# Kernel optimization log

Measured on AMD Instinct MI355X. Metric: run time of the kernel, lower is better.

Reference implementation:

```python
import jax, jax.numpy as jnp
import numpy as np

DECAY = 0.99
EPSILON = 1e-05


def setup_inputs() -> dict:
    key = jax.random.key(0)
    k1, k2, k3, k4 = jax.random.split(key, 4)
    B, S, D, K = 16, 2048, 512, 2048
    x = jax.random.normal(k1, (B, S, D), dtype=jnp.float32)
    embed = jax.random.normal(k2, (K, D), dtype=jnp.float32)
    cluster_size = jax.random.uniform(k3, (K,), dtype=jnp.float32)
    embed_avg = jax.random.normal(k4, (K, D), dtype=jnp.float32)
    return {"x": x, "embed": embed, "cluster_size": cluster_size, "embed_avg": embed_avg}


def reference(x, embed, cluster_size, embed_avg):
    # x: [B,S,D]  embed: [K,D]  cluster_size: [K]  embed_avg: [K,D]
    B, S, D = x.shape
    K = embed.shape[0]
    xf = x.reshape(-1, D)  # [N,D], N=B*S

    # quantize(): negative squared euclidean distance, argmax over codebook
    x_sq = jnp.sum(xf * xf, axis=1, keepdims=True)            # [N,1]
    e_sq = jnp.sum(embed * embed, axis=1)[None, :]            # [1,K]
    dist = -(x_sq - 2.0 * (xf @ embed.T) + e_sq)              # [N,K]
    embed_ind = jnp.argmax(dist, axis=-1)                     # [N] int

    # dequantize
    quantize = embed[embed_ind].reshape(B, S, D)

    # training EMA updates (onehot.sum(0) and x^T @ onehot expressed as segment sums)
    ones = jnp.ones((xf.shape[0],), dtype=x.dtype)
    bins = jax.ops.segment_sum(ones, embed_ind, num_segments=K)        # [K] == onehot.sum(0)
    embed_sum_t = jax.ops.segment_sum(xf, embed_ind, num_segments=K)   # [K,D] == (x.T @ onehot).T

    new_cluster_size = cluster_size * DECAY + (1.0 - DECAY) * bins
    new_embed_avg = embed_avg * DECAY + (1.0 - DECAY) * embed_sum_t

    total = new_cluster_size.sum()
    smoothed = (new_cluster_size + EPSILON) / (total + K * EPSILON) * total  # laplace smoothing
    new_embed = new_embed_avg / smoothed[:, None]

    return (quantize,
            embed_ind.reshape(B, S),
            dist.reshape(B, S, K),
            new_cluster_size,
            new_embed_avg,
            new_embed)
```

## Files before the change

### kernel.cpp

```cpp
#include <hip/hip_runtime.h>

#define DECAY 0.99f
#define OMD   0.01f
#define EPS   1e-5f

constexpr int Bb = 16, Ss = 2048, Dd = 512, Kk = 2048;
constexpr int Nn = Bb * Ss;

typedef __attribute__((ext_vector_type(8))) short short8;
typedef __attribute__((ext_vector_type(4))) float f32x4;

__device__ __forceinline__ unsigned short f2bf(float x) {
    unsigned u = __float_as_uint(x);
    unsigned r = (u + 0x7FFFu + ((u >> 16) & 1u)) >> 16;
    return (unsigned short)r;
}
__device__ __forceinline__ float bf2f(unsigned short u) {
    return __uint_as_float((unsigned)u << 16);
}

__device__ __forceinline__ void gload_lds16(const void* g, void* l) {
    __builtin_amdgcn_global_load_lds(
        (const __attribute__((address_space(1))) void*)g,
        (__attribute__((address_space(3))) void*)l, 16, 0, 0);
}

#define BARRIER() do { asm volatile("" ::: "memory"); \
                       __builtin_amdgcn_s_barrier();  \
                       asm volatile("" ::: "memory"); } while (0)

__global__ void rows_sq(const float* __restrict__ in, float* __restrict__ out, int nrows) {
    int row  = blockIdx.x * 4 + (threadIdx.x >> 6);
    int lane = threadIdx.x & 63;
    if (row >= nrows) return;
    const float4* p = (const float4*)(in + (size_t)row * Dd);
    float s = 0.f;
    #pragma unroll
    for (int i = 0; i < 2; ++i) {
        float4 v = p[lane + 64 * i];
        s += v.x * v.x + v.y * v.y + v.z * v.z + v.w * v.w;
    }
    #pragma unroll
    for (int off = 32; off; off >>= 1) s += __shfl_down(s, off);
    if (lane == 0) out[row] = s;
}

__global__ void conv_rows(const float* __restrict__ in,
                          unsigned short* __restrict__ ph,
                          unsigned short* __restrict__ pm,
                          float* __restrict__ sq) {
    int row  = blockIdx.x * 4 + (threadIdx.x >> 6);
    int lane = threadIdx.x & 63;
    const float4* p = (const float4*)(in + (size_t)row * Dd);
    ushort4* h4 = (ushort4*)(ph + (size_t)row * Dd);
    ushort4* m4 = (ushort4*)(pm + (size_t)row * Dd);
    float s = 0.f;
    #pragma unroll
    for (int i = 0; i < 2; ++i) {
        int idx = lane + 64 * i;
        float4 v = p[idx];
        float f[4] = {v.x, v.y, v.z, v.w};
        unsigned short hh[4], mm[4];
        #pragma unroll
        for (int j = 0; j < 4; ++j) {
            float x = f[j];
            s += x * x;
            unsigned short a = f2bf(x);
            unsigned short b = f2bf(x - bf2f(a));
            hh[j] = a; mm[j] = b;
        }
        h4[idx] = make_ushort4(hh[0], hh[1], hh[2], hh[3]);
        m4[idx] = make_ushort4(mm[0], mm[1], mm[2], mm[3]);
    }
    #pragma unroll
    for (int off = 32; off; off >>= 1) s += __shfl_down(s, off);
    if (lane == 0) sq[row] = s;
}

__global__ __launch_bounds__(512, 1) void gemm_split256(
    const unsigned short* __restrict__ xp,
    const unsigned short* __restrict__ ep,
    const float* __restrict__ xsq,
    const float* __restrict__ esq,
    float* __restrict__ dist,
    unsigned long long* __restrict__ packed)
{
    __shared__ unsigned short As[3][256][64];
    __shared__ unsigned short Bs[2][256][64];

    const int tid  = threadIdx.x;
    const int lane = tid & 63;
    const int wid  = tid >> 6;
    const int wr   = wid >> 2;
    const int wc   = wid & 3;

    int bid = blockIdx.x;
    int wg  = (bid & 7) * 128 + (bid >> 3);
    int mb  = wg >> 3, nb = wg & 7;
    const int row0 = mb * 256, col0 = nb * 256;

    f32x4 acc[8][4] = {};
    short8 af[4], afh[4], bl[2], blh[2], bh[2], bhh[2];

    const int l8   = lane >> 3;
    const int csrc = (lane & 7) ^ l8;

    auto Aplane = [&](int tt) -> const unsigned short* {
        int p = tt >> 3;
        return xp + (size_t)((p == 2 || p == 3) ? 1 : 0) * ((size_t)Nn * Dd);
    };
    auto Bplane = [&](int tt) -> const unsigned short* {
        int p = tt >> 3;
        return ep + (size_t)((p == 1 || p == 3) ? 1 : 0) * ((size_t)Kk * Dd);
    };

    auto stageAt = [&](const unsigned short* pl, int d, int tt) {
        int ko = (tt & 7) * 64;
        #pragma unroll
        for (int jj = 0; jj < 4; ++jj) {
            int rowbase = jj * 64 + wid * 8;
            const unsigned short* src =
                pl + (size_t)(row0 + rowbase + l8) * Dd + ko + csrc * 8;
            gload_lds16(src, &As[d][rowbase][0]);
        }
    };
    auto stageBt = [&](const unsigned short* pl, int d, int tt) {
        int ko = (tt & 7) * 64;
        #pragma unroll
        for (int jj = 0; jj < 4; ++jj) {
            int rowbase = jj * 64 + wid * 8;
            const unsigned short* src =
                pl + (size_t)(col0 + rowbase + l8) * Dd + ko + csrc * 8;
            gload_lds16(src, &Bs[d][rowbase][0]);
        }
    };

    auto readA4 = [&](int d, int msel) {
        #pragma unroll
        for (int m = 0; m < 4; ++m) {
            int r  = wr * 128 + (msel * 4 + m) * 16 + (lane & 15);
            int c  = ((lane >> 4))     ^ (r & 7);
            int c2 = ((lane >> 4) + 4) ^ (r & 7);
            af[m]  = *(const short8*)&As[d][r][c * 8];
            afh[m] = *(const short8*)&As[d][r][c2 * 8];
        }
    };
    auto readBlo = [&](int d) {
        #pragma unroll
        for (int n = 0; n < 2; ++n) {
            int r  = wc * 64 + n * 16 + (lane & 15);
            int c  = ((lane >> 4))     ^ (r & 7);
            int c2 = ((lane >> 4) + 4) ^ (r & 7);
            bl[n]  = *(const short8*)&Bs[d][r][c * 8];
            blh[n] = *(const short8*)&Bs[d][r][c2 * 8];
        }
    };
    auto readBhi = [&](int d) {
        #pragma unroll
        for (int n = 0; n < 2; ++n) {
            int r  = wc * 64 + (2 + n) * 16 + (lane & 15);
            int c  = ((lane >> 4))     ^ (r & 7);
            int c2 = ((lane >> 4) + 4) ^ (r & 7);
            bh[n]  = *(const short8*)&Bs[d][r][c * 8];
            bhh[n] = *(const short8*)&Bs[d][r][c2 * 8];
        }
    };

    auto mfmaQ = [&](int msel, int nsel, const short8* b0, const short8* b1) {
        #pragma unroll
        for (int m = 0; m < 4; ++m)
            #pragma unroll
            for (int n = 0; n < 2; ++n) {
                int am = msel * 4 + m, bn = nsel * 2 + n;
                acc[am][bn] = __builtin_amdgcn_mfma_f32_16x16x32_bf16(af[m], b0[n], acc[am][bn], 0, 0, 0);
            }
        #pragma unroll
        for (int m = 0; m < 4; ++m)
            #pragma unroll
            for (int n = 0; n < 2; ++n) {
                int am = msel * 4 + m, bn = nsel * 2 + n;
                acc[am][bn] = __builtin_amdgcn_mfma_f32_16x16x32_bf16(afh[m], b1[n], acc[am][bn], 0, 0, 0);
            }
    };

    stageAt(Aplane(0), 0, 0);
    stageBt(Bplane(0), 0, 0);
    stageAt(Aplane(1), 1, 1);
    asm volatile("s_waitcnt vmcnt(4)" ::: "memory");
    BARRIER();

    for (int t = 0; t < 32; ++t) {
        const int ca = t % 3, cb = t & 1;
        const int nbb = (t + 1) & 1;
        const int naa = (t + 2) % 3;

        stageBt(Bplane(t + 1), nbb, t + 1);
        stageAt(Aplane(t + 2), naa, t + 2);

        readA4(ca, 0); readBlo(cb); readBhi(cb);
        mfmaQ(0, 0, bl, blh);
        mfmaQ(0, 1, bh, bhh);
        readA4(ca, 1);
        mfmaQ(1, 1, bh, bhh);
        mfmaQ(1, 0, bl, blh);

        __builtin_amdgcn_sched_barrier(0);
        asm volatile("s_waitcnt vmcnt(4)" ::: "memory");
        BARRIER();
    }
    asm volatile("s_waitcnt vmcnt(0)" ::: "memory");

    const int jrow = (lane >> 4) * 4;
    const int ncol = lane & 15;
    #pragma unroll
    for (int m = 0; m < 8; ++m) {
        int rbase = row0 + wr * 128 + m * 16 + jrow;
        #pragma unroll
        for (int j = 0; j < 4; ++j) {
            int row = rbase + j;
            float xs = xsq[row];
            float best = -3.4e38f; int bi = 0;
            #pragma unroll
            for (int n = 0; n < 4; ++n) {
                int col = col0 + wc * 64 + n * 16 + ncol;
                float v = 2.f * acc[m][n][j] - xs - esq[col];
                dist[(size_t)row * Kk + col] = v;
                if (v > best) { best = v; bi = col; }
            }
            unsigned u = __float_as_uint(best);
            u = (u & 0x80000000u) ? ~u : (u | 0x80000000u);
            unsigned long long pk = ((unsigned long long)u << 32) | (unsigned)(~bi);
            #pragma unroll
            for (int off = 1; off < 16; off <<= 1) {
                unsigned long long o = __shfl_xor(pk, off);
                if (o > pk) pk = o;
            }
            if (ncol == 0) atomicMax(&packed[row], pk);
        }
    }
}

__global__ void gather_scatter_packed(const float* __restrict__ x,
                                      const float* __restrict__ embed,
                                      const unsigned long long* __restrict__ packed,
                                      float* __restrict__ quant,
                                      float* __restrict__ ind_f,
                                      float* __restrict__ esum,
                                      int* __restrict__ bins) {
    int n = blockIdx.x;
    int k = (int)(~(unsigned)(packed[n] & 0xFFFFFFFFull));
    int t = threadIdx.x;
    size_t xb = (size_t)n * Dd;
    size_t eb = (size_t)k * Dd;
    float v0 = x[xb + t];
    float v1 = x[xb + t + 256];
    quant[xb + t]       = embed[eb + t];
    quant[xb + t + 256] = embed[eb + t + 256];
    atomicAdd(&esum[eb + t],       v0);
    atomicAdd(&esum[eb + t + 256], v1);
    if (t == 0) { ind_f[n] = (float)k; atomicAdd(&bins[k], 1); }
}

#define BM 64
#define BN 64
#define BK 32
__global__ __launch_bounds__(256) void gemm_dist(
    const float* __restrict__ A, const float* __restrict__ Bm,
    const float* __restrict__ xsq, const float* __restrict__ esq,
    float* __restrict__ dist)
{
    __shared__ float Asl[BK][BM + 4];
    __shared__ float Bsl[BK][BN + 4];
    int tid = threadIdx.x;
    int row0 = blockIdx.x * BM, col0 = blockIdx.y * BN;
    int tx = tid & 15, ty = tid >> 4;
    float acc[4][4] = {};
    int lr = tid >> 3, lc = (tid & 7) * 4;
    for (int d0 = 0; d0 < Dd; d0 += BK) {
        float4 a0 = *(const float4*)(A  + (size_t)(row0 + lr)      * Dd + d0 + lc);
        float4 a1 = *(const float4*)(A  + (size_t)(row0 + lr + 32) * Dd + d0 + lc);
        float4 b0 = *(const float4*)(Bm + (size_t)(col0 + lr)      * Dd + d0 + lc);
        float4 b1 = *(const float4*)(Bm + (size_t)(col0 + lr + 32) * Dd + d0 + lc);
        __syncthreads();
        Asl[lc + 0][lr] = a0.x; Asl[lc + 1][lr] = a0.y; Asl[lc + 2][lr] = a0.z; Asl[lc + 3][lr] = a0.w;
        Asl[lc + 0][lr + 32] = a1.x; Asl[lc + 1][lr + 32] = a1.y; Asl[lc + 2][lr + 32] = a1.z; Asl[lc + 3][lr + 32] = a1.w;
        Bsl[lc + 0][lr] = b0.x; Bsl[lc + 1][lr] = b0.y; Bsl[lc + 2][lr] = b0.z; Bsl[lc + 3][lr] = b0.w;
        Bsl[lc + 0][lr + 32] = b1.x; Bsl[lc + 1][lr + 32] = b1.y; Bsl[lc + 2][lr + 32] = b1.z; Bsl[lc + 3][lr + 32] = b1.w;
        __syncthreads();
        #pragma unroll
        for (int kd = 0; kd < BK; ++kd) {
            float4 av = *(const float4*)&Asl[kd][ty * 4];
            float4 bv = *(const float4*)&Bsl[kd][tx * 4];
            float a[4] = {av.x, av.y, av.z, av.w};
            float b[4] = {bv.x, bv.y, bv.z, bv.w};
            #pragma unroll
            for (int i = 0; i < 4; ++i)
                #pragma unroll
                for (int j = 0; j < 4; ++j)
                    acc[i][j] = fmaf(a[i], b[j], acc[i][j]);
        }
    }
    #pragma unroll
    for (int i = 0; i < 4; ++i) {
        int row = row0 + ty * 4 + i;
        float xs = xsq[row];
        float4 o;
        int col = col0 + tx * 4;
        o.x = 2.f * acc[i][0] - xs - esq[col + 0];
        o.y = 2.f * acc[i][1] - xs - esq[col + 1];
        o.z = 2.f * acc[i][2] - xs - esq[col + 2];
        o.w = 2.f * acc[i][3] - xs - esq[col + 3];
        *(float4*)(dist + (size_t)row * Kk + col) = o;
    }
}

__global__ void argmax_k(const float* __restrict__ dist,
                         float* __restrict__ ind_f, int* __restrict__ ind_i) {
    int row  = blockIdx.x * 4 + (threadIdx.x >> 6);
    int lane = threadIdx.x & 63;
    const float4* p = (const float4*)(dist + (size_t)row * Kk);
    float best = -3.4e38f;
    int bidx = 0;
    #pragma unroll
    for (int it = 0; it < Kk / 4 / 64; ++it) {
        int i = lane + it * 64;
        float4 v = p[i];
        int base = i * 4;
        if (v.x > best) { best = v.x; bidx = base + 0; }
        if (v.y > best) { best = v.y; bidx = base + 1; }
        if (v.z > best) { best = v.z; bidx = base + 2; }
        if (v.w > best) { best = v.w; bidx = base + 3; }
    }
    #pragma unroll
    for (int off = 32; off; off >>= 1) {
        float ov = __shfl_down(best, off);
        int   oi = __shfl_down(bidx, off);
        if (ov > best || (ov == best && oi < bidx)) { best = ov; bidx = oi; }
    }
    if (lane == 0) { ind_f[row] = (float)bidx; ind_i[row] = bidx; }
}

__global__ void gather_scatter(const float* __restrict__ x,
                               const float* __restrict__ embed,
                               const int* __restrict__ ind,
                               float* __restrict__ quant,
                               float* __restrict__ esum,
                               int* __restrict__ bins) {
    int n = blockIdx.x;
    int k = ind[n];
    int t = threadIdx.x;
    size_t xb = (size_t)n * Dd;
    size_t eb = (size_t)k * Dd;
    float v0 = x[xb + t];
    float v1 = x[xb + t + 256];
    quant[xb + t]       = embed[eb + t];
    quant[xb + t + 256] = embed[eb + t + 256];
    atomicAdd(&esum[eb + t],       v0);
    atomicAdd(&esum[eb + t + 256], v1);
    if (t == 0) atomicAdd(&bins[k], 1);
}

__global__ void finalize1(const float* __restrict__ cs, const int* __restrict__ bins,
                          float* __restrict__ ncs, float* __restrict__ total_ws) {
    __shared__ float red[16];
    int t = threadIdx.x;
    float s = 0.f;
    for (int k = t; k < Kk; k += 1024) {
        float v = cs[k] * DECAY + OMD * (float)bins[k];
        ncs[k] = v;
        s += v;
    }
    #pragma unroll
    for (int off = 32; off; off >>= 1) s += __shfl_down(s, off);
    if ((t & 63) == 0) red[t >> 6] = s;
    __syncthreads();
    if (t == 0) {
        float tot = 0.f;
        #pragma unroll
        for (int i = 0; i < 16; ++i) tot += red[i];
        total_ws[0] = tot;
    }
}

__global__ void finalize2(const float* __restrict__ ea, const float* __restrict__ esum,
                          const float* __restrict__ ncs, const float* __restrict__ total_ws,
                          float* __restrict__ nea, float* __restrict__ ne) {
    int idx = blockIdx.x * 256 + threadIdx.x;
    float total = total_ws[0];
    int k = idx >> 7;
    float sm = (ncs[k] + EPS) / (total + Kk * EPS) * total;
    float inv = 1.f / sm;
    float4 a = ((const float4*)ea)[idx];
    float4 s = ((const float4*)esum)[idx];
    float4 r;
    r.x = a.x * DECAY + OMD * s.x;
    r.y = a.y * DECAY + OMD * s.y;
    r.z = a.z * DECAY + OMD * s.z;
    r.w = a.w * DECAY + OMD * s.w;
    ((float4*)nea)[idx] = r;
    float4 e;
    e.x = r.x * inv; e.y = r.y * inv; e.z = r.z * inv; e.w = r.w * inv;
    ((float4*)ne)[idx] = e;
}

extern "C" void kernel_launch(void* const* d_in, const int* in_sizes, int n_in,
                              void* d_out, int out_size, void* d_ws, size_t ws_size,
                              hipStream_t stream) {
    const float* x     = (const float*)d_in[0];
    const float* embed = (const float*)d_in[1];
    const float* cs    = (const float*)d_in[2];
    const float* ea    = (const float*)d_in[3];

    float* out     = (float*)d_out;
    float* o_quant = out;
    float* o_ind   = o_quant + (size_t)Nn * Dd;
    float* o_dist  = o_ind + Nn;
    float* o_ncs   = o_dist + (size_t)Nn * Kk;
    float* o_nea   = o_ncs + Kk;
    float* o_ne    = o_nea + (size_t)Kk * Dd;

    size_t xp_elems = (size_t)3 * Nn * Dd;
    size_t ep_elems = (size_t)3 * Kk * Dd;
    char* w = (char*)d_ws;
    unsigned short* xp = (unsigned short*)w;                 w += xp_elems * 2;
    unsigned short* epp = (unsigned short*)w;                w += ep_elems * 2;
    float* xsq   = (float*)w;                                w += (size_t)Nn * 4;
    float* esq   = (float*)w;                                w += (size_t)Kk * 4;
    int*   ind_i = (int*)w;                                  w += (size_t)Nn * 4;
    int*   bins  = (int*)w;                                  w += (size_t)Kk * 4;
    float* esum  = (float*)w;                                w += (size_t)Kk * Dd * 4;
    unsigned long long* packed = (unsigned long long*)w;     w += (size_t)Nn * 8;
    float* total = (float*)w;                                w += 256;
    size_t need = (size_t)(w - (char*)d_ws);

    if (ws_size >= need) {
        hipMemsetAsync(bins, 0, (size_t)Kk * 4 + (size_t)Kk * Dd * 4 + (size_t)Nn * 8, stream);

        conv_rows<<<Nn / 4, 256, 0, stream>>>(x, xp, xp + (size_t)Nn * Dd, xsq);
        conv_rows<<<Kk / 4, 256, 0, stream>>>(embed, epp, epp + (size_t)Kk * Dd, esq);

        gemm_split256<<<(Nn / 256) * (Kk / 256), 512, 0, stream>>>(
            xp, epp, xsq, esq, o_dist, packed);

        gather_scatter_packed<<<Nn, 256, 0, stream>>>(
            x, embed, packed, o_quant, o_ind, esum, bins);
    } else {
        float* fxsq  = (float*)d_ws;
        float* fesq  = fxsq + Nn;
        int*   find  = (int*)(fesq + Kk);
        int*   fbins = find + Nn;
        float* fesum = (float*)(fbins + Kk);
        float* ftot  = fesum + (size_t)Kk * Dd;
        xsq = fxsq; esq = fesq; ind_i = find; bins = fbins; esum = fesum; total = ftot;

        hipMemsetAsync(bins, 0, (size_t)(Kk + Kk * Dd) * sizeof(float), stream);
        rows_sq<<<Nn / 4, 256, 0, stream>>>(x, xsq, Nn);
        rows_sq<<<Kk / 4, 256, 0, stream>>>(embed, esq, Kk);
        dim3 g(Nn / BM, Kk / BN);
        gemm_dist<<<g, 256, 0, stream>>>(x, embed, xsq, esq, o_dist);
        argmax_k<<<Nn / 4, 256, 0, stream>>>(o_dist, o_ind, ind_i);
        gather_scatter<<<Nn, 256, 0, stream>>>(x, embed, ind_i, o_quant, esum, bins);
    }

    finalize1<<<1, 1024, 0, stream>>>(cs, bins, o_ncs, total);
    finalize2<<<(Kk * Dd / 4) / 256, 256, 0, stream>>>(ea, esum, o_ncs, total, o_nea, o_ne);
}
```

Baseline: 438.8 us.

## Fuse all four split-bf16 plane products per K tile in GEMM

Restructures the split-precision distance GEMM so each K step stages the hi and lo planes of both operands (32-wide) and issues all four cross products, instead of iterating over plane pairs with 64-wide tiles. This improves register fragment reuse across MFMAs and simplifies the loop to 16 double-buffered iterations. In exchange it waits for all loads each iteration, reducing prefetch depth, and uses a new swizzle for narrower LDS rows that may change bank conflict behaviour.

```diff
diff --git a/kernel.cpp b/kernel.cpp
--- a/kernel.cpp
+++ b/kernel.cpp
@@ -77,7 +77,7 @@
     if (lane == 0) sq[row] = s;
 }
 
-__global__ __launch_bounds__(512, 1) void gemm_split256(
+__global__ __launch_bounds__(512, 1) void gemm_fused4(
     const unsigned short* __restrict__ xp,
     const unsigned short* __restrict__ ep,
     const float* __restrict__ xsq,
@@ -85,8 +85,10 @@
     float* __restrict__ dist,
     unsigned long long* __restrict__ packed)
 {
-    __shared__ unsigned short As[3][256][64];
-    __shared__ unsigned short Bs[2][256][64];
+    __shared__ unsigned short Ah[2][256][32];
+    __shared__ unsigned short Am[2][256][32];
+    __shared__ unsigned short Bh[2][256][32];
+    __shared__ unsigned short Bm[2][256][32];
 
     const int tid  = threadIdx.x;
     const int lane = tid & 63;
@@ -100,115 +102,97 @@
     const int row0 = mb * 256, col0 = nb * 256;
 
     f32x4 acc[8][4] = {};
-    short8 af[4], afh[4], bl[2], blh[2], bh[2], bhh[2];
-
-    const int l8   = lane >> 3;
-    const int csrc = (lane & 7) ^ l8;
-
-    auto Aplane = [&](int tt) -> const unsigned short* {
-        int p = tt >> 3;
-        return xp + (size_t)((p == 2 || p == 3) ? 1 : 0) * ((size_t)Nn * Dd);
+
+    const unsigned short* xph = xp;
+    const unsigned short* xpm = xp + (size_t)Nn * Dd;
+    const unsigned short* eph = ep;
+    const unsigned short* epm = ep + (size_t)Kk * Dd;
+
+    auto stageP = [&](const unsigned short* pl, unsigned short (*dst)[32],
+                      int base, int ko) {
+        #pragma unroll
+        for (int jj = 0; jj < 2; ++jj) {
+            int rowbase = jj * 128 + wid * 16;
+            int row = rowbase + (lane >> 2);
+            int sc = (lane & 3) ^ ((row ^ (row >> 2)) & 3);
+            const unsigned short* src =
+                pl + (size_t)(base + row) * Dd + ko + sc * 8;
+            gload_lds16(src, &dst[rowbase][0]);
+        }
     };
-    auto Bplane = [&](int tt) -> const unsigned short* {
-        int p = tt >> 3;
-        return ep + (size_t)((p == 1 || p == 3) ? 1 : 0) * ((size_t)Kk * Dd);
+
+    auto readAfr = [&](unsigned short (*S)[32], int msel, short8* out) {
+        #pragma unroll
+        for (int m = 0; m < 4; ++m) {
+            int r = wr * 128 + (msel * 4 + m) * 16 + (lane & 15);
+            int c = (lane >> 4) ^ ((r ^ (r >> 2)) & 3);
+            out[m] = *(const short8*)&S[r][c * 8];
+        }
     };
-
-    auto stageAt = [&](const unsigned short* pl, int d, int tt) {
-        int ko = (tt & 7) * 64;
-        #pragma unroll
-        for (int jj = 0; jj < 4; ++jj) {
-            int rowbase = jj * 64 + wid * 8;
-            const unsigned short* src =
-                pl + (size_t)(row0 + rowbase + l8) * Dd + ko + csrc * 8;
-            gload_lds16(src, &As[d][rowbase][0]);
+    auto readBfr = [&](unsigned short (*S)[32], short8* out) {
+        #pragma unroll
+        for (int n = 0; n < 4; ++n) {
+            int r = wc * 64 + n * 16 + (lane & 15);
+            int c = (lane >> 4) ^ ((r ^ (r >> 2)) & 3);
+            out[n] = *(const short8*)&S[r][c * 8];
         }
     };
-    auto stageBt = [&](const unsigned short* pl, int d, int tt) {
-        int ko = (tt & 7) * 64;
-        #pragma unroll
-        for (int jj = 0; jj < 4; ++jj) {
-            int rowbase = jj * 64 + wid * 8;
-            const unsigned short* src =
-                pl + (size_t)(col0 + rowbase + l8) * Dd + ko + csrc * 8;
-            gload_lds16(src, &Bs[d][rowbase][0]);
-        }
-    };
-
-    auto readA4 = [&](int d, int msel) {
-        #pragma unroll
-        for (int m = 0; m < 4; ++m) {
-            int r  = wr * 128 + (msel * 4 + m) * 16 + (lane & 15);
-            int c  = ((lane >> 4))     ^ (r & 7);
-            int c2 = ((lane >> 4) + 4) ^ (r & 7);
-            af[m]  = *(const short8*)&As[d][r][c * 8];
-            afh[m] = *(const short8*)&As[d][r][c2 * 8];
-        }
-    };
-    auto readBlo = [&](int d) {
-        #pragma unroll
-        for (int n = 0; n < 2; ++n) {
-            int r  = wc * 64 + n * 16 + (lane & 15);
-            int c  = ((lane >> 4))     ^ (r & 7);
-            int c2 = ((lane >> 4) + 4) ^ (r & 7);
-            bl[n]  = *(const short8*)&Bs[d][r][c * 8];
-            blh[n] = *(const short8*)&Bs[d][r][c2 * 8];
-        }
-    };
-    auto readBhi = [&](int d) {
-        #pragma unroll
-        for (int n = 0; n < 2; ++n) {
-            int r  = wc * 64 + (2 + n) * 16 + (lane & 15);
-            int c  = ((lane >> 4))     ^ (r & 7);
-            int c2 = ((lane >> 4) + 4) ^ (r & 7);
-            bh[n]  = *(const short8*)&Bs[d][r][c * 8];
-            bhh[n] = *(const short8*)&Bs[d][r][c2 * 8];
-        }
-    };
-
-    auto mfmaQ = [&](int msel, int nsel, const short8* b0, const short8* b1) {
-        #pragma unroll
-        for (int m = 0; m < 4; ++m)
-            #pragma unroll
-            for (int n = 0; n < 2; ++n) {
-                int am = msel * 4 + m, bn = nsel * 2 + n;
-                acc[am][bn] = __builtin_amdgcn_mfma_f32_16x16x32_bf16(af[m], b0[n], acc[am][bn], 0, 0, 0);
-            }
-        #pragma unroll
-        for (int m = 0; m < 4; ++m)
-            #pragma unroll
-            for (int n = 0; n < 2; ++n) {
-                int am = msel * 4 + m, bn = nsel * 2 + n;
-                acc[am][bn] = __builtin_amdgcn_mfma_f32_16x16x32_bf16(afh[m], b1[n], acc[am][bn], 0, 0, 0);
-            }
-    };
-
-    stageAt(Aplane(0), 0, 0);
-    stageBt(Bplane(0), 0, 0);
-    stageAt(Aplane(1), 1, 1);
-    asm volatile("s_waitcnt vmcnt(4)" ::: "memory");
+
+    stageP(xph, Ah[0], row0, 0);
+    stageP(xpm, Am[0], row0, 0);
+    stageP(eph, Bh[0], col0, 0);
+    stageP(epm, Bm[0], col0, 0);
+    asm volatile("s_waitcnt vmcnt(0)" ::: "memory");
     BARRIER();
 
-    for (int t = 0; t < 32; ++t) {
-        const int ca = t % 3, cb = t & 1;
-        const int nbb = (t + 1) & 1;
-        const int naa = (t + 2) % 3;
-
-        stageBt(Bplane(t + 1), nbb, t + 1);
-        stageAt(Aplane(t + 2), naa, t + 2);
-
-        readA4(ca, 0); readBlo(cb); readBhi(cb);
-        mfmaQ(0, 0, bl, blh);
-        mfmaQ(0, 1, bh, bhh);
-        readA4(ca, 1);
-        mfmaQ(1, 1, bh, bhh);
-        mfmaQ(1, 0, bl, blh);
-
-        __builtin_amdgcn_sched_barrier(0);
-        asm volatile("s_waitcnt vmcnt(4)" ::: "memory");
+    for (int t = 0; t < 16; ++t) {
+        const int cur = t & 1, nxt = cur ^ 1;
+        if (t < 15) {
+            int kon = (t + 1) * 32;
+            stageP(xph, Ah[nxt], row0, kon);
+            stageP(xpm, Am[nxt], row0, kon);
+            stageP(eph, Bh[nxt], col0, kon);
+            stageP(epm, Bm[nxt], col0, kon);
+        }
+
+        short8 vbh[4], vbm[4];
+        readBfr(Bh[cur], vbh);
+        readBfr(Bm[cur], vbm);
+
+        #pragma unroll
+        for (int ms = 0; ms < 2; ++ms) {
+            short8 vah[4], vam[4];
+            readAfr(Ah[cur], ms, vah);
+            readAfr(Am[cur], ms, vam);
+            #pragma unroll
+            for (int m = 0; m < 4; ++m)
+                #pragma unroll
+                for (int n = 0; n < 4; ++n)
+                    acc[ms * 4 + m][n] = __builtin_amdgcn_mfma_f32_16x16x32_bf16(
+                        vah[m], vbh[n], acc[ms * 4 + m][n], 0, 0, 0);
+            #pragma unroll
+            for (int m = 0; m < 4; ++m)
+                #pragma unroll
+                for (int n = 0; n < 4; ++n)
+                    acc[ms * 4 + m][n] = __builtin_amdgcn_mfma_f32_16x16x32_bf16(
+                        vah[m], vbm[n], acc[ms * 4 + m][n], 0, 0, 0);
+            #pragma unroll
+            for (int m = 0; m < 4; ++m)
+                #pragma unroll
+                for (int n = 0; n < 4; ++n)
+                    acc[ms * 4 + m][n] = __builtin_amdgcn_mfma_f32_16x16x32_bf16(
+                        vam[m], vbh[n], acc[ms * 4 + m][n], 0, 0, 0);
+            #pragma unroll
+            for (int m = 0; m < 4; ++m)
+                #pragma unroll
+                for (int n = 0; n < 4; ++n)
+                    acc[ms * 4 + m][n] = __builtin_amdgcn_mfma_f32_16x16x32_bf16(
+                        vam[m], vbm[n], acc[ms * 4 + m][n], 0, 0, 0);
+        }
+
+        asm volatile("s_waitcnt vmcnt(0)" ::: "memory");
         BARRIER();
     }
-    asm volatile("s_waitcnt vmcnt(0)" ::: "memory");
 
     const int jrow = (lane >> 4) * 4;
     const int ncol = lane & 15;
@@ -265,7 +249,7 @@
 #define BN 64
 #define BK 32
 __global__ __launch_bounds__(256) void gemm_dist(
-    const float* __restrict__ A, const float* __restrict__ Bm,
+    const float* __restrict__ A, const float* __restrict__ Bm_,
     const float* __restrict__ xsq, const float* __restrict__ esq,
     float* __restrict__ dist)
 {
@@ -277,10 +261,10 @@
     float acc[4][4] = {};
     int lr = tid >> 3, lc = (tid & 7) * 4;
     for (int d0 = 0; d0 < Dd; d0 += BK) {
-        float4 a0 = *(const float4*)(A  + (size_t)(row0 + lr)      * Dd + d0 + lc);
-        float4 a1 = *(const float4*)(A  + (size_t)(row0 + lr + 32) * Dd + d0 + lc);
-        float4 b0 = *(const float4*)(Bm + (size_t)(col0 + lr)      * Dd + d0 + lc);
-        float4 b1 = *(const float4*)(Bm + (size_t)(col0 + lr + 32) * Dd + d0 + lc);
+        float4 a0 = *(const float4*)(A   + (size_t)(row0 + lr)      * Dd + d0 + lc);
+        float4 a1 = *(const float4*)(A   + (size_t)(row0 + lr + 32) * Dd + d0 + lc);
+        float4 b0 = *(const float4*)(Bm_ + (size_t)(col0 + lr)      * Dd + d0 + lc);
+        float4 b1 = *(const float4*)(Bm_ + (size_t)(col0 + lr + 32) * Dd + d0 + lc);
         __syncthreads();
         Asl[lc + 0][lr] = a0.x; Asl[lc + 1][lr] = a0.y; Asl[lc + 2][lr] = a0.z; Asl[lc + 3][lr] = a0.w;
         Asl[lc + 0][lr + 32] = a1.x; Asl[lc + 1][lr + 32] = a1.y; Asl[lc + 2][lr + 32] = a1.z; Asl[lc + 3][lr + 32] = a1.w;
@@ -439,7 +423,7 @@
         conv_rows<<<Nn / 4, 256, 0, stream>>>(x, xp, xp + (size_t)Nn * Dd, xsq);
         conv_rows<<<Kk / 4, 256, 0, stream>>>(embed, epp, epp + (size_t)Kk * Dd, esq);
 
-        gemm_split256<<<(Nn / 256) * (Kk / 256), 512, 0, stream>>>(
+        gemm_fused4<<<(Nn / 256) * (Kk / 256), 512, 0, stream>>>(
             xp, epp, xsq, esq, o_dist, packed);
 
         gather_scatter_packed<<<Nn, 256, 0, stream>>>(
```

Result: faster. 401.7 us (-8.4%).
